# Kernel optimization log

Measured on AMD Instinct MI355X. Metric: run time of the kernel, lower is better.

The kernel has to match this reference:

```python
import jax, jax.numpy as jnp
import numpy as np

B, S, D, H, L, FF, V = 2, 1024, 1024, 16, 4, 2048, 32000
DK = D // H
EPS = 1e-5  # torch LayerNorm default


def _pos_enc(n, d):
    # matches torch PositionalEncoding: pe[pos, 2i]=sin, pe[pos, 2i+1]=cos
    pos = jnp.arange(n, dtype=jnp.float32)[:, None]
    div = jnp.exp(jnp.arange(0, d, 2, dtype=jnp.float32) * (-jnp.log(10000.0) / d))
    pe = jnp.zeros((n, d), dtype=jnp.float32)
    pe = pe.at[:, 0::2].set(jnp.sin(pos * div))
    pe = pe.at[:, 1::2].set(jnp.cos(pos * div))
    return pe


def setup_inputs() -> dict:
    key = jax.random.key(0)
    ks = jax.random.split(key, 12)
    s = 0.02
    return {
        "tokens": jax.random.randint(ks[0], (B, S), 0, V, dtype=jnp.int32),
        "emb": jax.random.normal(ks[1], (V, D), jnp.float32) * s,
        "Wq": jax.random.normal(ks[2], (L, D, D), jnp.float32) * s,
        "bq": jnp.zeros((L, D), jnp.float32),
        "Wk": jax.random.normal(ks[3], (L, D, D), jnp.float32) * s,
        "bk": jnp.zeros((L, D), jnp.float32),
        "Wv": jax.random.normal(ks[4], (L, D, D), jnp.float32) * s,
        "bv": jnp.zeros((L, D), jnp.float32),
        "Wo": jax.random.normal(ks[5], (L, D, D), jnp.float32) * s,
        "bo": jnp.zeros((L, D), jnp.float32),
        "W1": jax.random.normal(ks[6], (L, D, FF), jnp.float32) * s,
        "b1": jnp.zeros((L, FF), jnp.float32),
        "W2": jax.random.normal(ks[7], (L, FF, D), jnp.float32) * s,
        "b2": jnp.zeros((L, D), jnp.float32),
        "gamma": jnp.ones((L, D), jnp.float32),
        "beta": jnp.zeros((L, D), jnp.float32),
    }


def _layernorm(x, g, b):
    mu = jnp.mean(x, axis=-1, keepdims=True)
    var = jnp.mean(jnp.square(x - mu), axis=-1, keepdims=True)
    return (x - mu) * jax.lax.rsqrt(var + EPS) * g + b


def _encoder_layer(x, p):
    Wq, bq, Wk, bk, Wv, bv, Wo, bo, W1, b1, W2, b2, g, be = p
    # naive MHA: explicit QK^T / softmax / AV, materializing [B,H,S,S]
    q = (x @ Wq + bq).reshape(B, S, H, DK).transpose(0, 2, 1, 3)
    k = (x @ Wk + bk).reshape(B, S, H, DK).transpose(0, 2, 1, 3)
    v = (x @ Wv + bv).reshape(B, S, H, DK).transpose(0, 2, 1, 3)
    scores = jnp.einsum("bhqd,bhkd->bhqk", q, k) / jnp.sqrt(jnp.float32(DK))
    attn = jax.nn.softmax(scores, axis=-1)
    o = jnp.einsum("bhqk,bhkd->bhqd", attn, v)
    o = o.transpose(0, 2, 1, 3).reshape(B, S, D) @ Wo + bo
    # NOTE: same LayerNorm params used twice, as in the original module
    x = _layernorm(x + o, g, be)
    f = jax.nn.relu(x @ W1 + b1) @ W2 + b2
    x = _layernorm(x + f, g, be)
    return x, None


def reference(tokens, emb, Wq, bq, Wk, bk, Wv, bv, Wo, bo, W1, b1, W2, b2, gamma, beta):
    x = emb[tokens]  # [B,S,D]
    # faithful to the original bug: pe[:x.size(0)] indexes the BATCH dim,
    # pe slice has shape [B,1,D] and broadcasts over the sequence dim
    x = x + _pos_enc(B, D)[:, None, :]
    params = (Wq, bq, Wk, bk, Wv, bv, Wo, bo, W1, b1, W2, b2, gamma, beta)
    x, _ = jax.lax.scan(_encoder_layer, x, params)
    return x
```

## Files before the change

kernel.cpp:

```cpp
#include <hip/hip_runtime.h>
#include <cstdint>
#include <cstddef>

#define Bx 2
#define Sx 1024
#define Dx 1024
#define Hx 16
#define Lx 4
#define FFx 2048
#define DKx 64
#define Mx (Bx * Sx)

typedef __attribute__((ext_vector_type(4))) float f32x4;
typedef __attribute__((ext_vector_type(8))) __bf16 bf16x8;
typedef __attribute__((ext_vector_type(4))) __bf16 bf16x4;
typedef __attribute__((ext_vector_type(2))) __bf16 bf16x2;

__global__ void embed_kernel(const int* __restrict__ tokens,
                             const float* __restrict__ emb,
                             float* __restrict__ x, __bf16* __restrict__ xb) {
  size_t i = (size_t)blockIdx.x * blockDim.x + threadIdx.x;
  if (i >= (size_t)Mx * Dx / 2) return;
  int p = (int)(i % (Dx / 2));
  size_t bs = i / (Dx / 2);
  int b = (int)(bs >> 10);
  int tok = tokens[bs];
  float arg = (float)b * expf((float)(2 * p) * (-logf(10000.0f) / (float)Dx));
  float sv, cv;
  __sincosf(arg, &sv, &cv);
  const float2 e = ((const float2*)(emb + (size_t)tok * Dx))[p];
  float2 o;
  o.x = e.x + sv;
  o.y = e.y + cv;
  ((float2*)x)[i] = o;
  bf16x2 ob;
  ob[0] = (__bf16)o.x;
  ob[1] = (__bf16)o.y;
  ((bf16x2*)xb)[i] = ob;
}

__global__ void transpose_to_bf16(const float* __restrict__ W, __bf16* __restrict__ Wt,
                                  int K, int N, size_t sstride, size_t dstride) {
  __shared__ float tile[32][33];
  const float* Ws = W + blockIdx.z * sstride;
  __bf16* Wd = Wt + blockIdx.z * dstride;
  int tx = threadIdx.x, ty = threadIdx.y;
  int n0 = blockIdx.x * 32, k0 = blockIdx.y * 32;
#pragma unroll
  for (int i = 0; i < 4; ++i)
    tile[ty + 8 * i][tx] = Ws[(size_t)(k0 + ty + 8 * i) * N + n0 + tx];
  __syncthreads();
#pragma unroll
  for (int i = 0; i < 4; ++i)
    Wd[(size_t)(n0 + ty + 8 * i) * K + k0 + tx] = (__bf16)tile[tx][ty + 8 * i];
}

struct T4Args {
  const float* s0; const float* s1; const float* s2; const float* s3;
  __bf16* d0; __bf16* d1; __bf16* d2; __bf16* d3;
};
__global__ void transpose4_to_bf16(T4Args a) {
  __shared__ float tile[32][33];
  const int zz = blockIdx.z, l = zz >> 2, which = zz & 3;
  const size_t M1c = (size_t)Dx * Dx;
  const float* Ws = (which == 0 ? a.s0 : which == 1 ? a.s1 : which == 2 ? a.s2 : a.s3) + (size_t)l * M1c;
  __bf16* Wd = (which == 0)   ? a.d0 + (size_t)l * 3 * M1c
               : (which == 1) ? a.d1 + (size_t)l * 3 * M1c
               : (which == 2) ? a.d2 + (size_t)l * 3 * M1c
                              : a.d3 + (size_t)l * M1c;
  int tx = threadIdx.x, ty = threadIdx.y;
  int n0 = blockIdx.x * 32, k0 = blockIdx.y * 32;
#pragma unroll
  for (int i = 0; i < 4; ++i)
    tile[ty + 8 * i][tx] = Ws[(size_t)(k0 + ty + 8 * i) * Dx + n0 + tx];
  __syncthreads();
#pragma unroll
  for (int i = 0; i < 4; ++i)
    Wd[(size_t)(n0 + ty + 8 * i) * Dx + k0 + tx] = (__bf16)tile[tx][ty + 8 * i];
}

__global__ void concat3_kernel(const float* __restrict__ a, const float* __restrict__ b,
                               const float* __restrict__ c, float* __restrict__ out) {
  int i = blockIdx.x * 256 + threadIdx.x;
  int l = i / 3072, j = i % 3072;
  float v = (j < 1024) ? a[l * 1024 + j]
                       : ((j < 2048) ? b[l * 1024 + j - 1024] : c[l * 1024 + j - 2048]);
  out[i] = v;
}

__device__ __forceinline__ void gld_lds16(const void* g, void* l) {
  __builtin_amdgcn_global_load_lds(
      (const __attribute__((address_space(1))) void*)(uintptr_t)g,
      (__attribute__((address_space(3))) void*)(uintptr_t)l, 16, 0, 0);
}

template <int TM, int TN, bool RELU, typename OutT, bool VOUT = false>
__global__ __launch_bounds__(256) void gemm_bt(const __bf16* __restrict__ A,
                                               const __bf16* __restrict__ Bt,
                                               const float* __restrict__ bias,
                                               OutT* __restrict__ C0,
                                               float* __restrict__ C1,
                                               __bf16* __restrict__ VT,
                                               int Kstep, int Kld, int ldc) {
  static_assert((TM + TN) == 192, "NCH fixed at 12");
  static_assert(!VOUT || TN == 64, "VOUT path assumes TN=64/WC=0");
  constexpr int LDSE = VOUT ? 64 * 136 : (TM + TN) * 32;
  __shared__ __align__(16) __bf16 lds[LDSE];
  const int t = threadIdx.x;
  const int w = t >> 6, lane = t & 63;
  const int quad = lane >> 4, l16 = lane & 15;
  const int m0 = blockIdx.y * TM, n0 = blockIdx.x * TN;
  const int lr = lane >> 2, lc = (lane & 3) * 8;
  const int koff = blockIdx.z * Kstep;

  f32x4 acc[2][4] = {};

  const int WR = (TN == 128) ? (w >> 1) * (TM / 2) : w * (TM / 4);
  const int WC = (TN == 128) ? (w & 1) * 64 : 0;
  const __bf16* Abase = A + (size_t)m0 * Kld + koff;
  const __bf16* Bbase = Bt + (size_t)n0 * Kld + koff;

  for (int k0 = 0; k0 < Kstep; k0 += 32) {
    __syncthreads();
#pragma unroll
    for (int c = 0; c < 3; ++c) {
      const int ch = c * 4 + w;
      const int r = ch * 16 + lr;
      const __bf16* g = (r < TM) ? (Abase + (size_t)r * Kld + k0 + lc)
                                 : (Bbase + (size_t)(r - TM) * Kld + k0 + lc);
      gld_lds16(g, (void*)(lds + ch * 512));
    }
    __syncthreads();
    bf16x8 af[2], bfr[4];
#pragma unroll
    for (int i = 0; i < 2; ++i)
      af[i] = *(const bf16x8*)&lds[(WR + i * 16 + l16) * 32 + quad * 8];
#pragma unroll
    for (int j = 0; j < 4; ++j)
      bfr[j] = *(const bf16x8*)&lds[(TM + WC + j * 16 + l16) * 32 + quad * 8];
#pragma unroll
    for (int i = 0; i < 2; ++i)
#pragma unroll
      for (int j = 0; j < 4; ++j)
        acc[i][j] = __builtin_amdgcn_mfma_f32_16x16x32_bf16(af[i], bfr[j], acc[i][j], 0, 0, 0);
  }

  const int col0 = n0 + WC + l16;

  if (VOUT && n0 >= 2048) {
    __syncthreads();
#pragma unroll
    for (int j = 0; j < 4; ++j) {
      const float bn = bias[col0 + j * 16];
      const int nl = (l16 + j * 16) * 136;
#pragma unroll
      for (int i = 0; i < 2; ++i)
#pragma unroll
        for (int r = 0; r < 4; ++r)
          lds[nl + WR + i * 16 + quad * 4 + r] = (__bf16)(acc[i][j][r] + bn);
    }
    __syncthreads();
    const int b = m0 >> 10;
    const int sbase = m0 & 1023;
    const int row = t >> 2, seg = t & 3;
    __bf16* vrow = VT + (size_t)(b * 1024 + (n0 - 2048) + row) * Sx + sbase + seg * 32;
    const __bf16* lrow = lds + row * 136 + seg * 32;
#pragma unroll
    for (int q = 0; q < 4; ++q)
      *(bf16x8*)(vrow + q * 8) = *(const bf16x8*)(lrow + q * 8);
    return;
  }

  const bool z0 = (blockIdx.z == 0);
#pragma unroll
  for (int j = 0; j < 4; ++j) {
    const int n = col0 + j * 16;
    const float bn = z0 ? bias[n] : 0.f;
#pragma unroll
    for (int i = 0; i < 2; ++i) {
#pragma unroll
      for (int r = 0; r < 4; ++r) {
        const int m = m0 + WR + i * 16 + quad * 4 + r;
        float v = acc[i][j][r] + bn;
        if (RELU) v = fmaxf(v, 0.f);
        if (z0)
          C0[(size_t)m * ldc + n] = (OutT)v;
        else
          C1[(size_t)m * ldc + n] = v;
      }
    }
  }
}

__global__ __launch_bounds__(256) void attention_mfma(const __bf16* __restrict__ QKV,
                                                      const __bf16* __restrict__ Vt,
                                                      __bf16* __restrict__ O) {
  __shared__ __align__(16) __bf16 Ks[2][64 * 72];
  __shared__ __align__(16) __bf16 Vs[2][64 * 72];
  __shared__ __align__(16) __bf16 Pl[64 * 72];

  const int t = threadIdx.x;
  const int w = t >> 6, lane = t & 63;
  const int quad = lane >> 4, l16 = lane & 15;
  const int q0 = blockIdx.x * 64;
  const int h = blockIdx.y, b = blockIdx.z;
  const size_t rowbase = (size_t)b * Sx;
  const int hoff = h * 64;

  const __bf16* qrow = QKV + (rowbase + q0 + w * 16 + l16) * 3072 + hoff;
  bf16x8 qf0 = *(const bf16x8*)(qrow + quad * 8);
  bf16x8 qf1 = *(const bf16x8*)(qrow + 32 + quad * 8);

  const __bf16* Kbase = QKV + rowbase * 3072 + 1024 + hoff;
  const __bf16* Vbase = Vt + (size_t)(b * Hx + h) * 64 * Sx;

  const int srow = t >> 2, sseg = t & 3;
  bf16x8 kp0, kp1, vp0, vp1;

  f32x4 oacc[4] = {};
  float lsum = 0.f;
  const float cs = 0.125f * 1.44269504089f;

  {
    const __bf16* kr = Kbase + (size_t)srow * 3072 + sseg * 16;
    kp0 = *(const bf16x8*)kr;
    kp1 = *(const bf16x8*)(kr + 8);
    const __bf16* vr = Vbase + (size_t)srow * Sx + sseg * 16;
    vp0 = *(const bf16x8*)vr;
    vp1 = *(const bf16x8*)(vr + 8);
    *(bf16x8*)&Ks[0][srow * 72 + sseg * 16] = kp0;
    *(bf16x8*)&Ks[0][srow * 72 + sseg * 16 + 8] = kp1;
    *(bf16x8*)&Vs[0][srow * 72 + sseg * 16] = vp0;
    *(bf16x8*)&Vs[0][srow * 72 + sseg * 16 + 8] = vp1;
  }
  __syncthreads();

  for (int kt = 0; kt < Sx / 64; ++kt) {
    const int cur = kt & 1;
    if (kt < Sx / 64 - 1) {
      const int kn = (kt + 1) * 64;
      const __bf16* kr = Kbase + (size_t)(kn + srow) * 3072 + sseg * 16;
      kp0 = *(const bf16x8*)kr;
      kp1 = *(const bf16x8*)(kr + 8);
      const __bf16* vr = Vbase + (size_t)srow * Sx + kn + sseg * 16;
      vp0 = *(const bf16x8*)vr;
      vp1 = *(const bf16x8*)(vr + 8);
    }

    f32x4 s[4] = {};
#pragma unroll
    for (int j = 0; j < 4; ++j) {
      bf16x8 b0 = *(const bf16x8*)&Ks[cur][(j * 16 + l16) * 72 + quad * 8];
      bf16x8 b1 = *(const bf16x8*)&Ks[cur][(j * 16 + l16) * 72 + 32 + quad * 8];
      s[j] = __builtin_amdgcn_mfma_f32_16x16x32_bf16(b0, qf0, s[j], 0, 0, 0);
      s[j] = __builtin_amdgcn_mfma_f32_16x16x32_bf16(b1, qf1, s[j], 0, 0, 0);
    }

#pragma unroll
    for (int j = 0; j < 4; ++j) {
#pragma unroll
      for (int r = 0; r < 4; ++r) s[j][r] = __builtin_exp2f(s[j][r] * cs);
      lsum += s[j][0] + s[j][1] + s[j][2] + s[j][3];
    }

    const int prow = (w * 16 + l16) * 72;
#pragma unroll
    for (int j = 0; j < 4; ++j) {
      bf16x4 pk;
#pragma unroll
      for (int r = 0; r < 4; ++r) pk[r] = (__bf16)s[j][r];
      *(bf16x4*)&Pl[prow + j * 16 + quad * 4] = pk;
    }
    bf16x8 pa0 = *(const bf16x8*)&Pl[prow + quad * 8];
    bf16x8 pa1 = *(const bf16x8*)&Pl[prow + 32 + quad * 8];

#pragma unroll
    for (int j = 0; j < 4; ++j) {
      bf16x8 vb0 = *(const bf16x8*)&Vs[cur][(j * 16 + l16) * 72 + quad * 8];
      bf16x8 vb1 = *(const bf16x8*)&Vs[cur][(j * 16 + l16) * 72 + 32 + quad * 8];
      oacc[j] = __builtin_amdgcn_mfma_f32_16x16x32_bf16(pa0, vb0, oacc[j], 0, 0, 0);
      oacc[j] = __builtin_amdgcn_mfma_f32_16x16x32_bf16(pa1, vb1, oacc[j], 0, 0, 0);
    }

    if (kt < Sx / 64 - 1) {
      const int nxt = 1 - cur;
      *(bf16x8*)&Ks[nxt][srow * 72 + sseg * 16] = kp0;
      *(bf16x8*)&Ks[nxt][srow * 72 + sseg * 16 + 8] = kp1;
      *(bf16x8*)&Vs[nxt][srow * 72 + sseg * 16] = vp0;
      *(bf16x8*)&Vs[nxt][srow * 72 + sseg * 16 + 8] = vp1;
    }
    __syncthreads();
  }

  lsum += __shfl_xor(lsum, 16);
  lsum += __shfl_xor(lsum, 32);
  const float inv = 1.f / lsum;
#pragma unroll
  for (int r = 0; r < 4; ++r) {
    const float invr = __shfl(inv, quad * 4 + r);
    const size_t orow = (rowbase + q0 + w * 16 + quad * 4 + r) * 1024 + hoff;
#pragma unroll
    for (int j = 0; j < 4; ++j) O[orow + j * 16 + l16] = (__bf16)(oacc[j][r] * invr);
  }
}

__global__ void add_ln_kernel(const float* __restrict__ x, const float* __restrict__ r0,
                              const float* __restrict__ r1,
                              const float* __restrict__ gamma, const float* __restrict__ beta,
                              float* __restrict__ out, __bf16* __restrict__ outb) {
  const int row = blockIdx.x, t = threadIdx.x;
  const int lane = t & 63, w = t >> 6;
  __shared__ float red[2][4];
  const f32x4* xr = (const f32x4*)(x + (size_t)row * Dx);
  const f32x4* a0 = (const f32x4*)(r0 + (size_t)row * Dx);
  const f32x4* a1 = (const f32x4*)(r1 + (size_t)row * Dx);
  f32x4 v = xr[t] + a0[t] + a1[t];
  float s = v[0] + v[1] + v[2] + v[3];
#pragma unroll
  for (int off = 1; off < 64; off <<= 1) s += __shfl_xor(s, off);
  if (lane == 0) red[0][w] = s;
  __syncthreads();
  const float mu = (red[0][0] + red[0][1] + red[0][2] + red[0][3]) * (1.f / Dx);
  f32x4 d = v - mu;
  float vs = d[0] * d[0] + d[1] * d[1] + d[2] * d[2] + d[3] * d[3];
#pragma unroll
  for (int off = 1; off < 64; off <<= 1) vs += __shfl_xor(vs, off);
  if (lane == 0) red[1][w] = vs;
  __syncthreads();
  const float is = rsqrtf((red[1][0] + red[1][1] + red[1][2] + red[1][3]) * (1.f / Dx) + 1e-5f);
  f32x4 g = ((const f32x4*)gamma)[t];
  f32x4 be = ((const f32x4*)beta)[t];
  f32x4 y = d * is * g + be;
  ((f32x4*)(out + (size_t)row * Dx))[t] = y;
  bf16x4 yb;
#pragma unroll
  for (int r = 0; r < 4; ++r) yb[r] = (__bf16)y[r];
  ((bf16x4*)(outb + (size_t)row * Dx))[t] = yb;
}

extern "C" void kernel_launch(void* const* d_in, const int* in_sizes, int n_in,
                              void* d_out, int out_size, void* d_ws, size_t ws_size,
                              hipStream_t stream) {
  const int* tokens = (const int*)d_in[0];
  const float* emb = (const float*)d_in[1];
  const float* Wq = (const float*)d_in[2];
  const float* bq = (const float*)d_in[3];
  const float* Wk = (const float*)d_in[4];
  const float* bk = (const float*)d_in[5];
  const float* Wv = (const float*)d_in[6];
  const float* bv = (const float*)d_in[7];
  const float* Wo = (const float*)d_in[8];
  const float* bo = (const float*)d_in[9];
  const float* W1 = (const float*)d_in[10];
  const float* b1 = (const float*)d_in[11];
  const float* W2 = (const float*)d_in[12];
  const float* b2 = (const float*)d_in[13];
  const float* gamma = (const float*)d_in[14];
  const float* beta = (const float*)d_in[15];

  const size_t M1 = 1024 * 1024;
  float* ws = (float*)d_ws;
  float* x = ws;
  float* tmp = ws + 2 * M1;
  __bf16* bfr = (__bf16*)(ws + 4 * M1);
  __bf16* xb = bfr;
  __bf16* qkvb = bfr + 2 * M1;
  __bf16* ob = bfr + 8 * M1;
  __bf16* h1b = bfr + 10 * M1;
  __bf16* Vt = bfr + 14 * M1;
  __bf16* WqkvT = bfr + 16 * M1;
  __bf16* WoT = bfr + 28 * M1;
  __bf16* W1T = bfr + 32 * M1;
  __bf16* W2T = bfr + 40 * M1;
  float* bqkv = (float*)(bfr + 48 * M1);
  float* tmp1 = (float*)qkvb;

  embed_kernel<<<((size_t)Mx * Dx / 2 + 255) / 256, 256, 0, stream>>>(tokens, emb, x, xb);

  dim3 tb(32, 8);
  T4Args t4{Wq, Wk, Wv, Wo, WqkvT, WqkvT + M1, WqkvT + 2 * M1, WoT};
  transpose4_to_bf16<<<dim3(32, 32, 4 * Lx), tb, 0, stream>>>(t4);
  transpose_to_bf16<<<dim3(64, 32, Lx), tb, 0, stream>>>(W1, W1T, Dx, FFx, 2 * M1, 2 * M1);
  transpose_to_bf16<<<dim3(32, 64, Lx), tb, 0, stream>>>(W2, W2T, FFx, Dx, 2 * M1, 2 * M1);
  concat3_kernel<<<Lx * 12, 256, 0, stream>>>(bq, bk, bv, bqkv);

  for (int l = 0; l < Lx; ++l) {
    const __bf16* WqkvT_l = WqkvT + (size_t)l * 3 * M1;
    const __bf16* WoT_l = WoT + (size_t)l * M1;
    const __bf16* W1T_l = W1T + (size_t)l * 2 * M1;
    const __bf16* W2T_l = W2T + (size_t)l * 2 * M1;
    const float* bqkv_l = bqkv + (size_t)l * 3072;
    const float* bo_l = bo + (size_t)l * Dx;
    const float* b1_l = b1 + (size_t)l * FFx;
    const float* b2_l = b2 + (size_t)l * Dx;
    const float* g_l = gamma + (size_t)l * Dx;
    const float* be_l = beta + (size_t)l * Dx;

    gemm_bt<128, 64, false, __bf16, true><<<dim3(3072 / 64, Mx / 128, 1), 256, 0, stream>>>(
        xb, WqkvT_l, bqkv_l, qkvb, nullptr, Vt, Dx, Dx, 3072);

    attention_mfma<<<dim3(Sx / 64, Hx, Bx), 256, 0, stream>>>(qkvb, Vt, ob);

    gemm_bt<64, 128, false, float><<<dim3(Dx / 128, Mx / 64, 2), 256, 0, stream>>>(
        ob, WoT_l, bo_l, tmp, tmp1, nullptr, Dx / 2, Dx, Dx);
    add_ln_kernel<<<Mx, 256, 0, stream>>>(x, tmp, tmp1, g_l, be_l, x, xb);

    gemm_bt<128, 64, true, __bf16><<<dim3(FFx / 64, Mx / 128, 1), 256, 0, stream>>>(
        xb, W1T_l, b1_l, h1b, nullptr, nullptr, Dx, Dx, FFx);
    gemm_bt<64, 128, false, float><<<dim3(Dx / 128, Mx / 64, 2), 256, 0, stream>>>(
        h1b, W2T_l, b2_l, tmp, tmp1, nullptr, FFx / 2, FFx, Dx);
    add_ln_kernel<<<Mx, 256, 0, stream>>>(x, tmp, tmp1, g_l, be_l,
                                          (l == Lx - 1) ? (float*)d_out : x, xb);
  }
}
```

Measured before the change: 793.3 us.

## Double-buffer GEMM LDS staging and add XCD-aware block swizzle

The GEMM kernel now keeps two LDS buffers and issues the global-to-LDS loads for the next K tile before computing on the current one, leaving one barrier per iteration instead of two. The GEMM and attention kernels also remap workgroup indices so that consecutive tiles land on the same XCD, aiming for better L2 reuse. Costs: double LDS footprint, which can lower occupancy. The VOUT epilogue reuses the flat buffer, which the diff assumes fits in 2*192*32 elements. The global_load_lds writes issued for the next tile may not be waited on correctly by the single barrier, so there is some correctness risk around async completion.

```diff
diff --git a/kernel.cpp b/kernel.cpp
--- a/kernel.cpp
+++ b/kernel.cpp
@@ -88,6 +88,14 @@
   out[i] = v;
 }
 
+__device__ __forceinline__ void xcd_swz_xy(int& bx, int& by) {
+  const int nwg = gridDim.x * gridDim.y;
+  int flat = by * gridDim.x + bx;
+  flat = (flat & 7) * (nwg >> 3) + (flat >> 3);
+  bx = flat % gridDim.x;
+  by = flat / gridDim.x;
+}
+
 __device__ __forceinline__ void gld_lds16(const void* g, void* l) {
   __builtin_amdgcn_global_load_lds(
       (const __attribute__((address_space(1))) void*)(uintptr_t)g,
@@ -104,12 +112,13 @@
                                                int Kstep, int Kld, int ldc) {
   static_assert((TM + TN) == 192, "NCH fixed at 12");
   static_assert(!VOUT || TN == 64, "VOUT path assumes TN=64/WC=0");
-  constexpr int LDSE = VOUT ? 64 * 136 : (TM + TN) * 32;
-  __shared__ __align__(16) __bf16 lds[LDSE];
+  __shared__ __align__(16) __bf16 lds[2][(TM + TN) * 32];
   const int t = threadIdx.x;
   const int w = t >> 6, lane = t & 63;
   const int quad = lane >> 4, l16 = lane & 15;
-  const int m0 = blockIdx.y * TM, n0 = blockIdx.x * TN;
+  int bx = blockIdx.x, by = blockIdx.y;
+  xcd_swz_xy(bx, by);
+  const int m0 = by * TM, n0 = bx * TN;
   const int lr = lane >> 2, lc = (lane & 3) * 8;
   const int koff = blockIdx.z * Kstep;
 
@@ -120,35 +129,43 @@
   const __bf16* Abase = A + (size_t)m0 * Kld + koff;
   const __bf16* Bbase = Bt + (size_t)n0 * Kld + koff;
 
-  for (int k0 = 0; k0 < Kstep; k0 += 32) {
-    __syncthreads();
+  auto stage = [&](int buf, int k0) {
 #pragma unroll
     for (int c = 0; c < 3; ++c) {
       const int ch = c * 4 + w;
       const int r = ch * 16 + lr;
       const __bf16* g = (r < TM) ? (Abase + (size_t)r * Kld + k0 + lc)
                                  : (Bbase + (size_t)(r - TM) * Kld + k0 + lc);
-      gld_lds16(g, (void*)(lds + ch * 512));
-    }
-    __syncthreads();
+      gld_lds16(g, (void*)(&lds[buf][0] + ch * 512));
+    }
+  };
+
+  stage(0, 0);
+  __syncthreads();
+
+  int cur = 0;
+  for (int k0 = 0; k0 < Kstep; k0 += 32) {
+    if (k0 + 32 < Kstep) stage(cur ^ 1, k0 + 32);
     bf16x8 af[2], bfr[4];
 #pragma unroll
     for (int i = 0; i < 2; ++i)
-      af[i] = *(const bf16x8*)&lds[(WR + i * 16 + l16) * 32 + quad * 8];
+      af[i] = *(const bf16x8*)&lds[cur][(WR + i * 16 + l16) * 32 + quad * 8];
 #pragma unroll
     for (int j = 0; j < 4; ++j)
-      bfr[j] = *(const bf16x8*)&lds[(TM + WC + j * 16 + l16) * 32 + quad * 8];
+      bfr[j] = *(const bf16x8*)&lds[cur][(TM + WC + j * 16 + l16) * 32 + quad * 8];
 #pragma unroll
     for (int i = 0; i < 2; ++i)
 #pragma unroll
       for (int j = 0; j < 4; ++j)
         acc[i][j] = __builtin_amdgcn_mfma_f32_16x16x32_bf16(af[i], bfr[j], acc[i][j], 0, 0, 0);
+    __syncthreads();
+    cur ^= 1;
   }
 
   const int col0 = n0 + WC + l16;
 
   if (VOUT && n0 >= 2048) {
-    __syncthreads();
+    __bf16* ldsf = &lds[0][0];
 #pragma unroll
     for (int j = 0; j < 4; ++j) {
       const float bn = bias[col0 + j * 16];
@@ -157,14 +174,14 @@
       for (int i = 0; i < 2; ++i)
 #pragma unroll
         for (int r = 0; r < 4; ++r)
-          lds[nl + WR + i * 16 + quad * 4 + r] = (__bf16)(acc[i][j][r] + bn);
+          ldsf[nl + WR + i * 16 + quad * 4 + r] = (__bf16)(acc[i][j][r] + bn);
     }
     __syncthreads();
     const int b = m0 >> 10;
     const int sbase = m0 & 1023;
     const int row = t >> 2, seg = t & 3;
     __bf16* vrow = VT + (size_t)(b * 1024 + (n0 - 2048) + row) * Sx + sbase + seg * 32;
-    const __bf16* lrow = lds + row * 136 + seg * 32;
+    const __bf16* lrow = ldsf + row * 136 + seg * 32;
 #pragma unroll
     for (int q = 0; q < 4; ++q)
       *(bf16x8*)(vrow + q * 8) = *(const bf16x8*)(lrow + q * 8);
@@ -202,8 +219,10 @@
   const int t = threadIdx.x;
   const int w = t >> 6, lane = t & 63;
   const int quad = lane >> 4, l16 = lane & 15;
-  const int q0 = blockIdx.x * 64;
-  const int h = blockIdx.y, b = blockIdx.z;
+  int bx = blockIdx.x, by = blockIdx.y;
+  xcd_swz_xy(bx, by);
+  const int q0 = bx * 64;
+  const int h = by, b = blockIdx.z;
   const size_t rowbase = (size_t)b * Sx;
   const int hoff = h * 64;
 
```

Measured after the change: 749.0 us. -5.6%, faster.
